# Kernel tuning notes

Hardware: AMD Instinct MI355X
Metric: run time of the kernel (lower is better)

The kernel has to match this reference:

```python
import jax, jax.numpy as jnp
import numpy as np
import math

B, L, HID = 2, 1024, 1536
NH, HD = 24, 64
DSSM = NH * HD            # 1536 (expand = 1)
QKV = 3 * DSSM
DCONV = 2
EPS = 1e-6


def _silu(u):
    return u * jax.nn.sigmoid(u)


def setup_inputs() -> dict:
    key = jax.random.key(0)
    ks = jax.random.split(key, 10)
    x = jax.random.normal(ks[0], (B, L, HID), dtype=jnp.float32)
    w_qkv = jax.random.normal(ks[1], (QKV, HID), dtype=jnp.float32) / math.sqrt(HID)
    conv_w = jax.random.normal(ks[2], (QKV, DCONV), dtype=jnp.float32) * 0.5  # depthwise causal conv, k=2
    w_dt = jax.random.normal(ks[3], (NH, HID), dtype=jnp.float32) * 0.02
    # dt_bias init exactly as in the torch module
    dt = jnp.exp(jax.random.uniform(ks[4], (NH,)) * (math.log(0.1) - math.log(0.001)) + math.log(0.001))
    dt = jnp.clip(dt, 1e-4, None)
    dt_bias = dt + jnp.log(-jnp.expm1(-dt))
    a_log = jnp.log(jax.random.uniform(ks[5], (NH,), minval=1.0, maxval=16.0))
    D = jnp.ones((NH, HD), dtype=jnp.float32)
    w_z = jax.random.normal(ks[6], (DSSM, HID), dtype=jnp.float32) / math.sqrt(HID)
    b_z = jnp.zeros((DSSM,), dtype=jnp.float32)
    rms_w = jnp.ones((DSSM,), dtype=jnp.float32)
    w_o = jax.random.normal(ks[7], (HID, DSSM), dtype=jnp.float32) / math.sqrt(DSSM)
    return dict(x=x, w_qkv=w_qkv, conv_w=conv_w, w_dt=w_dt, dt_bias=dt_bias,
                a_log=a_log, D=D, w_z=w_z, b_z=b_z, rms_w=rms_w, w_o=w_o)


def reference(x, w_qkv, conv_w, w_dt, dt_bias, a_log, D, w_z, b_z, rms_w, w_o):
    # qkv projection  [B,L,3*DSSM]
    qkv = jnp.einsum('blh,qh->blq', x, w_qkv)
    # depthwise causal conv1d (kernel size 2, padding k-1, trimmed to L)
    prev = jnp.pad(qkv, ((0, 0), (1, 0), (0, 0)))[:, :L]
    qkv = _silu(prev * conv_w[:, 0] + qkv * conv_w[:, 1])
    q, k, v = jnp.split(qkv, 3, axis=-1)
    q = q.reshape(B, L, NH, HD)
    k = k.reshape(B, L, NH, HD)
    v = v.reshape(B, L, NH, HD)
    # dt discretization: softplus(dt_proj(x) + dt_bias)   [B,L,NH]
    dt = jax.nn.softplus(jnp.einsum('blh,nh->bln', x, w_dt) + dt_bias)
    A = -jnp.exp(a_log)              # [NH], negative
    dA = dt * A                      # [B,L,NH]
    cs = jnp.transpose(jnp.cumsum(dA, axis=1), (0, 2, 1))   # [B,NH,L]
    diff = cs[:, :, :, None] - cs[:, :, None, :]            # [B,NH,L,L], <=0 on causal part
    causal = jnp.tril(jnp.ones((L, L), dtype=bool))
    decay = jnp.exp(jnp.where(causal, diff, -jnp.inf))      # segment-sum decay matrix
    # quadratic SSD (attention) form of the selective scan
    scores = jnp.einsum('bihd,bjhd->bhij', q, k) * decay
    scores = scores * jnp.transpose(dt, (0, 2, 1))[:, :, None, :]  # dt_j on keys (B-discretization)
    y = jnp.einsum('bhij,bjhd->bihd', scores, v)
    y = y + v * D                    # D skip connection
    y = y.reshape(B, L, DSSM)
    # z gate + RMSNorm + output projection
    z = jnp.einsum('blh,dh->bld', x, w_z) + b_z
    y = y * _silu(z)
    y = y * jax.lax.rsqrt(jnp.mean(y * y, axis=-1, keepdims=True) + EPS) * rms_w
    return jnp.einsum('bld,hd->blh', y, w_o)
```

## Files before the change

kernel.cpp:

```cpp
#include <hip/hip_runtime.h>
#include <hip/hip_bf16.h>
#include <math.h>

#define B_ 2
#define L_ 1024
#define HID_ 1536
#define NH_ 24
#define HD_ 64
#define DSSM_ 1536
#define QKV_ 4608
#define M_ 2048

typedef __attribute__((ext_vector_type(8))) short short8;
typedef __attribute__((ext_vector_type(4))) short short4e;
typedef __attribute__((ext_vector_type(4))) float floatx4;

__device__ __forceinline__ void gload_lds16(const short* g, short* l)
{
    __builtin_amdgcn_global_load_lds(
        (const __attribute__((address_space(1))) void*)g,
        (__attribute__((address_space(3))) void*)l,
        16, 0, 0);
}

__device__ __forceinline__ float bfs2f(short s)
{
    unsigned u = ((unsigned)(unsigned short)s) << 16;
    float f; __builtin_memcpy(&f, &u, 4); return f;
}
__device__ __forceinline__ short f2bfs(float f)
{
    __hip_bfloat16 h = __float2bfloat16(f);
    short s; __builtin_memcpy(&s, &h, 2); return s;
}

__device__ const int kIt[30] = {0,1,2,3,4,5, 6,6, 7,7, 8,8, 9,9, 10,10, 11,11,
                                12,12,12, 13,13,13, 14,14,14, 15,15,15};
__device__ const int kS[30]  = {0,0,0,0,0,0, 0,1, 0,1, 0,1, 0,1, 0,1, 0,1,
                                0,1,2, 0,1,2, 0,1,2, 0,1,2};

#define CN0 (M_ * HID_)
#define CN1 (QKV_ * HID_)
#define CN2 (DSSM_ * HID_)
#define CN3 (HID_ * DSSM_)
__global__ void cast_all_kernel(
    const float* __restrict__ x,  const float* __restrict__ wq,
    const float* __restrict__ wz, const float* __restrict__ wo,
    __hip_bfloat16* __restrict__ xb,
    __hip_bfloat16* __restrict__ wcat,
    __hip_bfloat16* __restrict__ wob)
{
    int i = (blockIdx.x * 256 + threadIdx.x) * 4;
    const float* src; __hip_bfloat16* dst; int off;
    if (i < CN0)                   { src = x;  dst = xb;         off = i; }
    else if (i < CN0 + CN1)        { src = wq; dst = wcat;       off = i - CN0; }
    else if (i < CN0 + CN1 + CN2)  { src = wz; dst = wcat + CN1; off = i - CN0 - CN1; }
    else                           { src = wo; dst = wob;        off = i - CN0 - CN1 - CN2; }
    float4 f = *reinterpret_cast<const float4*>(src + off);
    dst[off]     = __float2bfloat16(f.x);
    dst[off + 1] = __float2bfloat16(f.y);
    dst[off + 2] = __float2bfloat16(f.z);
    dst[off + 3] = __float2bfloat16(f.w);
}

#define MFMA_ __builtin_amdgcn_mfma_f32_16x16x32_bf16
#define BAR_() __builtin_amdgcn_s_barrier()

#define CSTR 200

__global__ __launch_bounds__(512, 1) void gemm_qkvz_256(
    const __hip_bfloat16* __restrict__ A,
    const __hip_bfloat16* __restrict__ Bm,
    __hip_bfloat16* __restrict__ qkv_out,
    float* __restrict__ z_out,
    const float* __restrict__ b_z)
{
    extern __shared__ short lds[];
    const int K  = HID_;
    const int NT = K / 64;
    const int tid   = threadIdx.x;
    const int lane  = tid & 63;
    const int wave  = tid >> 6;
    const int col16 = lane & 15;
    const int quad  = lane >> 4;
    const int wm = wave >> 1;
    const int wn = wave & 1;
    const int rowblk = blockIdx.y * 256;
    const int colblk = blockIdx.x * 192;

    const short* Ap = reinterpret_cast<const short*>(A);
    const short* Bp = reinterpret_cast<const short*>(Bm);

    const int o  = tid * 16;
    const int s  = o ^ (((o >> 7) & 7) << 4);
    const int sr = s >> 7;
    const int sc = (s & 127) >> 1;
    const int ldst = tid * 8;

    const int mask = (col16 & 7) << 4;
    const int e0 = ((quad * 16)      ^ mask) >> 1;
    const int e1 = ((64 + quad * 16) ^ mask) >> 1;
    const int arow = (wm * 64 + col16) * 64;
    const int brow = (wn * 96 + col16) * 64;

    floatx4 acc[4][6] = {};

    auto STAGE_A = [&](int c, int u, int t) {
        const short* g = Ap + (size_t)(rowblk + u * 64 + sr) * K + t * 64 + sc;
        gload_lds16(g, &lds[c * 16384 + u * 4096 + ldst]);
    };
    auto STAGE_B = [&](int c, int u, int t) {
        const short* g = Bp + (size_t)(colblk + u * 64 + sr) * K + t * 64 + sc;
        gload_lds16(g, &lds[32768 + c * 12288 + u * 4096 + ldst]);
    };

    STAGE_A(0, 0, 0); STAGE_A(0, 1, 0); STAGE_A(0, 2, 0); STAGE_A(0, 3, 0);
    STAGE_B(0, 0, 0); STAGE_B(0, 1, 0); STAGE_B(0, 2, 0);
    STAGE_A(1, 0, 1); STAGE_A(1, 1, 1); STAGE_A(1, 2, 1); STAGE_A(1, 3, 1);
    asm volatile("s_waitcnt vmcnt(4)" ::: "memory");
    __builtin_amdgcn_sched_barrier(0);
    BAR_();

    for (int t = 0; t < NT; ++t) {
        const int cur = t & 1, nxt = cur ^ 1;
        const int Ab = cur * 16384;
        const int Bb = 32768 + cur * 12288;
        short8 af0[4], af1[4], bf0[6], bf1[6];

#pragma unroll
        for (int m = 0; m < 4; ++m) {
            af0[m] = *reinterpret_cast<const short8*>(&lds[Ab + arow + m * 1024 + e0]);
            af1[m] = *reinterpret_cast<const short8*>(&lds[Ab + arow + m * 1024 + e1]);
        }
#pragma unroll
        for (int n = 0; n < 6; ++n) {
            bf0[n] = *reinterpret_cast<const short8*>(&lds[Bb + brow + n * 1024 + e0]);
            bf1[n] = *reinterpret_cast<const short8*>(&lds[Bb + brow + n * 1024 + e1]);
        }
        asm volatile("s_waitcnt lgkmcnt(0)" ::: "memory");
        __builtin_amdgcn_sched_barrier(0);
        BAR_();

        if (t + 1 < NT) {
            STAGE_B(nxt, 0, t + 1); STAGE_B(nxt, 1, t + 1); STAGE_B(nxt, 2, t + 1);
        }
        if (t + 2 < NT) {
            STAGE_A(cur, 0, t + 2); STAGE_A(cur, 1, t + 2);
            STAGE_A(cur, 2, t + 2); STAGE_A(cur, 3, t + 2);
        }

        __builtin_amdgcn_s_setprio(1);
#pragma unroll
        for (int m = 0; m < 4; ++m)
#pragma unroll
            for (int n = 0; n < 6; ++n) {
                acc[m][n] = MFMA_(af0[m], bf0[n], acc[m][n], 0, 0, 0);
                acc[m][n] = MFMA_(af1[m], bf1[n], acc[m][n], 0, 0, 0);
            }
        __builtin_amdgcn_s_setprio(0);

        if (t >= NT - 2) { asm volatile("s_waitcnt vmcnt(0)" ::: "memory"); }
        else             { asm volatile("s_waitcnt vmcnt(4)" ::: "memory"); }
        __builtin_amdgcn_sched_barrier(0);
        BAR_();
    }

    if (blockIdx.x < 24) {
        const int rb = wm * 64 + quad * 4;
        const int cb = wn * 96 + col16;
#pragma unroll
        for (int m = 0; m < 4; ++m)
#pragma unroll
            for (int n = 0; n < 6; ++n)
#pragma unroll
                for (int r = 0; r < 4; ++r)
                    lds[(rb + m * 16 + r) * CSTR + cb + n * 16] =
                        f2bfs(acc[m][n][r]);
        __syncthreads();
        const int row = tid >> 1;
        const int seg = tid & 1;
        const short* srcp = &lds[row * CSTR + seg * 96];
        short* dstp = reinterpret_cast<short*>(qkv_out)
                    + (size_t)(rowblk + row) * QKV_ + colblk + seg * 96;
#pragma unroll
        for (int j = 0; j < 12; ++j)
            *reinterpret_cast<short8*>(dstp + j * 8) =
                *reinterpret_cast<const short8*>(srcp + j * 8);
    } else {
        const int row0  = rowblk + wm * 64;
        const int col0g = colblk + wn * 96 - QKV_;
#pragma unroll
        for (int m = 0; m < 4; ++m)
#pragma unroll
            for (int n = 0; n < 6; ++n)
#pragma unroll
                for (int r = 0; r < 4; ++r) {
                    int row = row0 + m * 16 + quad * 4 + r;
                    int col = col0g + n * 16 + col16;
                    z_out[(size_t)row * DSSM_ + col] = acc[m][n][r] + b_z[col];
                }
    }
}

template<int OUTMODE>
__global__ __launch_bounds__(256) void gemm_nt(
    const __hip_bfloat16* __restrict__ A,
    const __hip_bfloat16* __restrict__ Bm,
    void* __restrict__ Cv,
    const float* __restrict__ bias,
    int M, int N, int K)
{
    const int lane  = threadIdx.x & 63;
    const int wave  = threadIdx.x >> 6;
    const int col16 = lane & 15;
    const int quad  = lane >> 4;
    const int wr    = wave >> 1;
    const int wc    = wave & 1;
    const int rowblk = blockIdx.y * 128;
    const int colblk = blockIdx.x * 128;

    const short* Ap = reinterpret_cast<const short*>(A);
    const short* Bp = reinterpret_cast<const short*>(Bm);

    __shared__ alignas(16) short As[128 * 32];
    __shared__ alignas(16) short Bs[128 * 32];

    const int srow = lane >> 2;
    const int scol = (lane & 3) * 8;

    floatx4 acc[4][4] = {};

    for (int k0 = 0; k0 < K; k0 += 32) {
#pragma unroll
        for (int s2 = 0; s2 < 2; ++s2) {
            const int seg = wave * 2 + s2;
            gload_lds16(Ap + (size_t)(rowblk + seg * 16 + srow) * K + k0 + scol,
                        &As[seg * 512]);
            gload_lds16(Bp + (size_t)(colblk + seg * 16 + srow) * K + k0 + scol,
                        &Bs[seg * 512]);
        }
        __syncthreads();

        short8 af[4], bf[4];
#pragma unroll
        for (int t = 0; t < 4; ++t) {
            af[t] = *reinterpret_cast<const short8*>(
                &As[(wr * 64 + t * 16 + col16) * 32 + quad * 8]);
            bf[t] = *reinterpret_cast<const short8*>(
                &Bs[(wc * 64 + t * 16 + col16) * 32 + quad * 8]);
        }
#pragma unroll
        for (int mt = 0; mt < 4; ++mt)
#pragma unroll
            for (int nt = 0; nt < 4; ++nt)
                acc[mt][nt] = __builtin_amdgcn_mfma_f32_16x16x32_bf16(
                    af[mt], bf[nt], acc[mt][nt], 0, 0, 0);
        __syncthreads();
    }

    const int row0 = rowblk + wr * 64;
    const int col0 = colblk + wc * 64;
#pragma unroll
    for (int mt = 0; mt < 4; ++mt) {
#pragma unroll
        for (int nt = 0; nt < 4; ++nt) {
#pragma unroll
            for (int r = 0; r < 4; ++r) {
                int row = row0 + mt * 16 + quad * 4 + r;
                int col = col0 + nt * 16 + col16;
                float v = acc[mt][nt][r];
                if (OUTMODE == 1) v += bias[col];
                if (OUTMODE == 2)
                    ((__hip_bfloat16*)Cv)[(size_t)row * N + col] = __float2bfloat16(v);
                else
                    ((float*)Cv)[(size_t)row * N + col] = v;
            }
        }
    }
}

__global__ void conv_silu_kernel(
    const __hip_bfloat16* __restrict__ raw,
    const float* __restrict__ conv_w,
    __hip_bfloat16* __restrict__ q,
    __hip_bfloat16* __restrict__ k,
    __hip_bfloat16* __restrict__ v)
{
    int idx8 = blockIdx.x * 256 + threadIdx.x;
    int c8 = (idx8 % (QKV_ / 8)) * 8;
    int ml = idx8 / (QKV_ / 8);
    int l  = ml % L_;
    int b  = ml / L_;

    const short* base = reinterpret_cast<const short*>(raw) + (size_t)ml * QKV_ + c8;
    short8 curv = *reinterpret_cast<const short8*>(base);
    short8 prevv = {};
    if (l > 0) prevv = *reinterpret_cast<const short8*>(base - QKV_);

    float4 w0 = *reinterpret_cast<const float4*>(conv_w + c8 * 2);
    float4 w1 = *reinterpret_cast<const float4*>(conv_w + c8 * 2 + 4);
    float4 w2 = *reinterpret_cast<const float4*>(conv_w + c8 * 2 + 8);
    float4 w3 = *reinterpret_cast<const float4*>(conv_w + c8 * 2 + 12);
    const float wa[16] = {w0.x, w0.y, w0.z, w0.w, w1.x, w1.y, w1.z, w1.w,
                          w2.x, w2.y, w2.z, w2.w, w3.x, w3.y, w3.z, w3.w};

    short8 outv;
#pragma unroll
    for (int j = 0; j < 8; ++j) {
        float u = bfs2f(prevv[j]) * wa[2 * j] + bfs2f(curv[j]) * wa[2 * j + 1];
        u = fmaxf(u, -80.f);
        outv[j] = f2bfs(u / (1.f + __expf(-u)));
    }

    int part = c8 / DSSM_;
    int cc   = c8 % DSSM_;
    int nh   = cc >> 6;
    int d    = cc & 63;
    __hip_bfloat16* dst = (part == 0) ? q : ((part == 1) ? k : v);
    *reinterpret_cast<short8*>(
        reinterpret_cast<short*>(dst) + (((size_t)b * NH_ + nh) * L_ + l) * HD_ + d)
        = outv;
}

__global__ __launch_bounds__(256) void dtproj_kernel(
    const float* __restrict__ x,
    const float* __restrict__ w_dt,
    const float* __restrict__ dt_bias,
    const float* __restrict__ a_log,
    float* __restrict__ dt,
    float* __restrict__ dA)
{
    const int tid  = threadIdx.x;
    const int wave = tid >> 6;
    const int lane = tid & 63;
    const int m0   = blockIdx.x * 8 + wave * 2;

    float4 xa[2][6];
#pragma unroll
    for (int rr = 0; rr < 2; ++rr)
#pragma unroll
        for (int j = 0; j < 6; ++j)
            xa[rr][j] = *reinterpret_cast<const float4*>(
                x + (size_t)(m0 + rr) * HID_ + lane * 4 + j * 256);

    float acc0[NH_], acc1[NH_];
#pragma unroll
    for (int n = 0; n < NH_; ++n) {
        float s0 = 0.f, s1 = 0.f;
#pragma unroll
        for (int j = 0; j < 6; ++j) {
            float4 w = *reinterpret_cast<const float4*>(
                w_dt + (size_t)n * HID_ + lane * 4 + j * 256);
            s0 += xa[0][j].x * w.x + xa[0][j].y * w.y
                + xa[0][j].z * w.z + xa[0][j].w * w.w;
            s1 += xa[1][j].x * w.x + xa[1][j].y * w.y
                + xa[1][j].z * w.z + xa[1][j].w * w.w;
        }
        acc0[n] = s0;
        acc1[n] = s1;
    }

#pragma unroll
    for (int off = 32; off; off >>= 1) {
#pragma unroll
        for (int n = 0; n < NH_; ++n) {
            acc0[n] += __shfl_xor(acc0[n], off, 64);
            acc1[n] += __shfl_xor(acc1[n], off, 64);
        }
    }

    if (lane < NH_) {
        const int n = lane;
        float bias = dt_bias[n];
        float Aval = -__expf(a_log[n]);
        float v0 = acc0[n] + bias;
        float v1 = acc1[n] + bias;
        v0 = (v0 > 20.f) ? v0 : log1pf(__expf(v0));
        v1 = (v1 > 20.f) ? v1 : log1pf(__expf(v1));
        int b0 = m0 / L_, l0 = m0 % L_;
        size_t o0 = ((size_t)b0 * NH_ + n) * L_ + l0;
        dt[o0]     = v0;
        dA[o0]     = v0 * Aval;
        dt[o0 + 1] = v1;
        dA[o0 + 1] = v1 * Aval;
    }
}

__global__ void cumsum_kernel(const float* __restrict__ dA, float* __restrict__ cs)
{
    int bnh  = blockIdx.x;
    int lane = threadIdx.x;
    const float* src = dA + (size_t)bnh * L_;
    float* dst       = cs + (size_t)bnh * L_;

    float loc[16];
    float run = 0.f;
#pragma unroll
    for (int t = 0; t < 16; ++t) { run += src[lane * 16 + t]; loc[t] = run; }
    float tot = run;
    float sc = tot;
#pragma unroll
    for (int off = 1; off < 64; off <<= 1) {
        float o = __shfl_up(sc, off, 64);
        if (lane >= off) sc += o;
    }
    float offset = sc - tot;
#pragma unroll
    for (int t = 0; t < 16; ++t) dst[lane * 16 + t] = loc[t] + offset;
}

__global__ __launch_bounds__(256) void vdt_transpose_kernel(
    const __hip_bfloat16* __restrict__ v,
    const float* __restrict__ dt,
    __hip_bfloat16* __restrict__ vt)
{
    const int lt0 = blockIdx.x * 64;
    const int bnh = blockIdx.z * NH_ + blockIdx.y;
    const int tid = threadIdx.x;

    __shared__ short T[64][72];

    {
        int row = tid >> 2;
        int cc  = (tid & 3) * 16;
        const short* sp = reinterpret_cast<const short*>(v)
                        + ((size_t)bnh * L_ + lt0 + row) * HD_ + cc;
        float dtr = dt[(size_t)bnh * L_ + lt0 + row];
        short8 a = *reinterpret_cast<const short8*>(sp);
        short8 b = *reinterpret_cast<const short8*>(sp + 8);
#pragma unroll
        for (int j = 0; j < 8; ++j) {
            T[row][cc + j]     = f2bfs(bfs2f(a[j]) * dtr);
            T[row][cc + 8 + j] = f2bfs(bfs2f(b[j]) * dtr);
        }
    }
    __syncthreads();
    {
        int d  = tid >> 2;
        int lc = (tid & 3) * 16;
        short8 o0, o1;
#pragma unroll
        for (int j = 0; j < 8; ++j) {
            o0[j] = T[lc + j][d];
            o1[j] = T[lc + 8 + j][d];
        }
        short* dst = reinterpret_cast<short*>(vt)
                   + ((size_t)bnh * HD_ + d) * L_ + lt0 + lc;
        *reinterpret_cast<short8*>(dst)     = o0;
        *reinterpret_cast<short8*>(dst + 8) = o1;
    }
}

__global__ __launch_bounds__(256) void attn_kernel(
    const __hip_bfloat16* __restrict__ q,
    const __hip_bfloat16* __restrict__ k,
    const __hip_bfloat16* __restrict__ vt,
    const float* __restrict__ cs,
    float* __restrict__ p0,
    float* __restrict__ p1,
    float* __restrict__ p2)
{
    const int pidx = blockIdx.x;
    const int it   = kIt[pidx];
    const int sl   = kS[pidx];
    const int nh   = blockIdx.y;
    const int b    = blockIdx.z;
    const int tid  = threadIdx.x;
    const int lane = tid & 63;
    const int wave = tid >> 6;
    const int col  = lane & 15;
    const int quad = lane >> 4;
    const int bnh  = b * NH_ + nh;
    const int iw0  = it * 64 + wave * 16;

    float* pout = (sl == 0) ? p0 : ((sl == 1) ? p1 : p2);

    const short* qp  = reinterpret_cast<const short*>(q);
    const short* kp  = reinterpret_cast<const short*>(k);
    const short* vtp = reinterpret_cast<const short*>(vt);

    __shared__ alignas(16) short Ks[4096];
    __shared__ alignas(16) short Ps[4 * 16 * 72];

    const short* qrow = qp + ((size_t)bnh * L_ + iw0 + col) * HD_;
    short8 aq0 = *reinterpret_cast<const short8*>(qrow + quad * 8);
    short8 aq1 = *reinterpret_cast<const short8*>(qrow + 32 + quad * 8);

    float csr[4];
#pragma unroll
    for (int r = 0; r < 4; ++r)
        csr[r] = cs[(size_t)bnh * L_ + iw0 + quad * 4 + r];

    floatx4 accO[4] = {};

    const int jt_end = min(sl * 6 + 5, it);
    for (int jt = sl * 6; jt <= jt_end; ++jt) {
        const int j0 = jt * 64;
        {
            const short* gk = kp + ((size_t)bnh * L_ + j0 + wave * 16 + (lane >> 2)) * HD_
                            + (lane & 3) * 8;
            gload_lds16(gk,      &Ks[wave * 512 + lane * 8]);
            gload_lds16(gk + 32, &Ks[2048 + wave * 512 + lane * 8]);
        }
        __syncthreads();

#pragma unroll
        for (int s = 0; s < 4; ++s) {
            int jsub = j0 + s * 16;
            if (jsub <= iw0 + 15) {
                short8 bk0 = *reinterpret_cast<const short8*>(
                    &Ks[(s * 16 + col) * 32 + quad * 8]);
                short8 bk1 = *reinterpret_cast<const short8*>(
                    &Ks[2048 + (s * 16 + col) * 32 + quad * 8]);
                floatx4 sc = {};
                sc = __builtin_amdgcn_mfma_f32_16x16x32_bf16(aq0, bk0, sc, 0, 0, 0);
                sc = __builtin_amdgcn_mfma_f32_16x16x32_bf16(aq1, bk1, sc, 0, 0, 0);
                int j = jsub + col;
                float csj = cs[(size_t)bnh * L_ + j];
#pragma unroll
                for (int r = 0; r < 4; ++r) {
                    int i = iw0 + quad * 4 + r;
                    float e = (j <= i) ? __expf(csr[r] - csj) : 0.f;
                    Ps[wave * 1152 + (quad * 4 + r) * 72 + s * 16 + col] =
                        f2bfs(sc[r] * e);
                }
            } else if (j0 + (s >> 1) * 32 <= iw0 + 15) {
#pragma unroll
                for (int r = 0; r < 4; ++r)
                    Ps[wave * 1152 + (quad * 4 + r) * 72 + s * 16 + col] = 0;
            }
        }

#pragma unroll
        for (int c = 0; c < 2; ++c) {
            if (j0 + c * 32 > iw0 + 15) continue;
            short8 pa = *reinterpret_cast<const short8*>(
                &Ps[wave * 1152 + col * 72 + c * 32 + quad * 8]);
#pragma unroll
            for (int nt = 0; nt < 4; ++nt) {
                short8 bv = *reinterpret_cast<const short8*>(
                    vtp + ((size_t)bnh * HD_ + nt * 16 + col) * L_
                        + j0 + c * 32 + quad * 8);
                accO[nt] = __builtin_amdgcn_mfma_f32_16x16x32_bf16(pa, bv, accO[nt], 0, 0, 0);
            }
        }
        __syncthreads();
    }

#pragma unroll
    for (int nt = 0; nt < 4; ++nt) {
#pragma unroll
        for (int r = 0; r < 4; ++r) {
            int i  = iw0 + quad * 4 + r;
            int dv = nt * 16 + col;
            pout[((size_t)b * L_ + i) * DSSM_ + nh * HD_ + dv] = accO[nt][r];
        }
    }
}

__global__ __launch_bounds__(256) void gate_rms_kernel(
    const float* __restrict__ p0,
    const float* __restrict__ p1,
    const float* __restrict__ p2,
    const float* __restrict__ z,
    const __hip_bfloat16* __restrict__ v,
    const float* __restrict__ Dm,
    const float* __restrict__ rms_w,
    __hip_bfloat16* __restrict__ yn)
{
    int m   = blockIdx.x;
    int b   = m / L_;
    int l   = m % L_;
    int tid = threadIdx.x;
    size_t base = (size_t)m * DSSM_;
    const bool has1 = (l >= 384);
    const bool has2 = (l >= 768);

    floatx4 acc4[2] = {};
    float ss = 0.f;
#pragma unroll
    for (int t = 0; t < 2; ++t) {
        int i4 = t * 256 + tid;
        if (i4 < DSSM_ / 4) {
            int c  = i4 * 4;
            int nh = c >> 6, d = c & 63;
            floatx4 p = *reinterpret_cast<const floatx4*>(p0 + base + c);
            if (has1) p += *reinterpret_cast<const floatx4*>(p1 + base + c);
            if (has2) p += *reinterpret_cast<const floatx4*>(p2 + base + c);
            floatx4 dm = *reinterpret_cast<const floatx4*>(Dm + c);
            floatx4 zz = *reinterpret_cast<const floatx4*>(z + base + c);
            short4e vv = *reinterpret_cast<const short4e*>(
                reinterpret_cast<const short*>(v)
                + (((size_t)b * NH_ + nh) * L_ + l) * HD_ + d);
            floatx4 g;
#pragma unroll
            for (int j = 0; j < 4; ++j) {
                float yv = p[j] + bfs2f(vv[j]) * dm[j];
                float zv = fmaxf(zz[j], -80.f);
                float gv = yv * (zv / (1.f + __expf(-zv)));
                ss += gv * gv;
                g[j] = gv;
            }
            acc4[t] = g;
        }
    }
#pragma unroll
    for (int off = 32; off; off >>= 1) ss += __shfl_xor(ss, off, 64);
    __shared__ float red[4];
    if ((tid & 63) == 0) red[tid >> 6] = ss;
    __syncthreads();
    ss = red[0] + red[1] + red[2] + red[3];
    float r = rsqrtf(ss / (float)DSSM_ + 1e-6f);
#pragma unroll
    for (int t = 0; t < 2; ++t) {
        int i4 = t * 256 + tid;
        if (i4 < DSSM_ / 4) {
            int c = i4 * 4;
            floatx4 rw = *reinterpret_cast<const floatx4*>(rms_w + c);
            short4e o;
#pragma unroll
            for (int j = 0; j < 4; ++j)
                o[j] = f2bfs(acc4[t][j] * r * rw[j]);
            *reinterpret_cast<short4e*>(
                reinterpret_cast<short*>(yn) + base + c) = o;
        }
    }
}

extern "C" void kernel_launch(void* const* d_in, const int* in_sizes, int n_in,
                              void* d_out, int out_size, void* d_ws, size_t ws_size,
                              hipStream_t stream)
{
    const float* x       = (const float*)d_in[0];
    const float* w_qkv   = (const float*)d_in[1];
    const float* conv_w  = (const float*)d_in[2];
    const float* w_dt    = (const float*)d_in[3];
    const float* dt_bias = (const float*)d_in[4];
    const float* a_log   = (const float*)d_in[5];
    const float* Dm      = (const float*)d_in[6];
    const float* w_z     = (const float*)d_in[7];
    const float* b_z     = (const float*)d_in[8];
    const float* rms_w   = (const float*)d_in[9];
    const float* w_o     = (const float*)d_in[10];
    float* out = (float*)d_out;

    char* ws = (char*)d_ws;

    __hip_bfloat16* xb    = (__hip_bfloat16*)(ws);
    __hip_bfloat16* wob   = (__hip_bfloat16*)(ws + 6291456);
    float*          zbuf  = (float*)(ws + 11010048);
    __hip_bfloat16* wcat  = (__hip_bfloat16*)(ws + 23592960);
    __hip_bfloat16* qkvb  = (__hip_bfloat16*)(ws + 42467328);
    __hip_bfloat16* qb    = (__hip_bfloat16*)(ws + 61341696);
    __hip_bfloat16* kb    = (__hip_bfloat16*)(ws + 67633152);
    __hip_bfloat16* vb    = (__hip_bfloat16*)(ws + 73924608);
    float* dt   = (float*)(ws + 80216064);
    float* dA   = (float*)(ws + 80412672);
    float* cs   = (float*)(ws + 80609280);
    __hip_bfloat16* vtb = (__hip_bfloat16*)(ws);
    __hip_bfloat16* yn  = (__hip_bfloat16*)(ws);
    float* p0 = (float*)(ws + 23592960);
    float* p1 = (float*)(ws + 36175872);
    float* p2 = (float*)(ws + 48758784);

    static bool attr_set = false;
    if (!attr_set) {
        (void)hipFuncSetAttribute(reinterpret_cast<const void*>(gemm_qkvz_256),
                                  hipFuncAttributeMaxDynamicSharedMemorySize,
                                  114688);
        attr_set = true;
    }

    cast_all_kernel<<<(CN0 + CN1 + CN2 + CN3) / 1024, 256, 0, stream>>>(
        x, w_qkv, w_z, w_o, xb, wcat, wob);

    gemm_qkvz_256<<<dim3((QKV_ + DSSM_) / 192, M_ / 256), 512, 114688, stream>>>(
        xb, wcat, qkvb, zbuf, b_z);

    conv_silu_kernel<<<(B_ * L_ * QKV_ / 8) / 256, 256, 0, stream>>>(
        qkvb, conv_w, qb, kb, vb);

    dtproj_kernel<<<M_ / 8, 256, 0, stream>>>(x, w_dt, dt_bias, a_log, dt, dA);

    cumsum_kernel<<<B_ * NH_, 64, 0, stream>>>(dA, cs);

    vdt_transpose_kernel<<<dim3(L_ / 64, NH_, B_), 256, 0, stream>>>(vb, dt, vtb);

    attn_kernel<<<dim3(30, NH_, B_), 256, 0, stream>>>(
        qb, kb, vtb, cs, p0, p1, p2);

    gate_rms_kernel<<<M_, 256, 0, stream>>>(p0, p1, p2, zbuf, vb, Dm, rms_w, yn);

    gemm_nt<0><<<dim3(HID_ / 128, M_ / 128), 256, 0, stream>>>(
        yn, wob, (void*)out, nullptr, M_, HID_, DSSM_);
}
```

Baseline: 276.2 us.

## Software-pipeline LDS fragment reads with MFMA halves in QKVZ GEMM

Restructures the QKVZ GEMM main loop so each K-tile's two 32-wide halves are read from LDS into separate register fragment sets, with the next half's LDS reads issued before the current half's MFMA cluster. A and B tiles for step t+2 are now staged together into the same buffer, and the wait counts are adjusted to match. The goal is to hide LDS read latency behind MFMA work. In exchange it adds an extra barrier per iteration and keeps two fragment sets live, which raises register pressure.

```diff
diff --git a/kernel.cpp b/kernel.cpp
--- a/kernel.cpp
+++ b/kernel.cpp
@@ -65,8 +65,32 @@
 
 #define MFMA_ __builtin_amdgcn_mfma_f32_16x16x32_bf16
 #define BAR_() __builtin_amdgcn_s_barrier()
+#define SCHED_ __builtin_amdgcn_sched_barrier(0)
 
 #define CSTR 200
+
+#define READ_FRAGS(Ab, Bb, eoff, fa, fb)                                        \
+    do {                                                                        \
+        _Pragma("unroll")                                                       \
+        for (int m_ = 0; m_ < 4; ++m_)                                          \
+            fa[m_] = *reinterpret_cast<const short8*>(                          \
+                &lds[(Ab) + arow + m_ * 1024 + (eoff)]);                        \
+        _Pragma("unroll")                                                       \
+        for (int n_ = 0; n_ < 6; ++n_)                                          \
+            fb[n_] = *reinterpret_cast<const short8*>(                          \
+                &lds[(Bb) + brow + n_ * 1024 + (eoff)]);                        \
+    } while (0)
+
+#define MFMA_CLUSTER(fa, fb)                                                    \
+    do {                                                                        \
+        __builtin_amdgcn_s_setprio(1);                                          \
+        _Pragma("unroll")                                                       \
+        for (int m_ = 0; m_ < 4; ++m_)                                          \
+            _Pragma("unroll")                                                   \
+            for (int n_ = 0; n_ < 6; ++n_)                                      \
+                acc[m_][n_] = MFMA_(fa[m_], fb[n_], acc[m_][n_], 0, 0, 0);      \
+        __builtin_amdgcn_s_setprio(0);                                          \
+    } while (0)
 
 __global__ __launch_bounds__(512, 1) void gemm_qkvz_256(
     const __hip_bfloat16* __restrict__ A,
@@ -105,64 +129,59 @@
 
     floatx4 acc[4][6] = {};
 
-    auto STAGE_A = [&](int c, int u, int t) {
-        const short* g = Ap + (size_t)(rowblk + u * 64 + sr) * K + t * 64 + sc;
-        gload_lds16(g, &lds[c * 16384 + u * 4096 + ldst]);
+    auto STAGE_ALL = [&](int c, int t) {
+        const short* ga = Ap + (size_t)(rowblk + sr) * K + t * 64 + sc;
+        short* da = &lds[c * 16384 + ldst];
+#pragma unroll
+        for (int u = 0; u < 4; ++u)
+            gload_lds16(ga + (size_t)(u * 64) * K, da + u * 4096);
+        const short* gb = Bp + (size_t)(colblk + sr) * K + t * 64 + sc;
+        short* db = &lds[32768 + c * 12288 + ldst];
+#pragma unroll
+        for (int u = 0; u < 3; ++u)
+            gload_lds16(gb + (size_t)(u * 64) * K, db + u * 4096);
     };
-    auto STAGE_B = [&](int c, int u, int t) {
-        const short* g = Bp + (size_t)(colblk + u * 64 + sr) * K + t * 64 + sc;
-        gload_lds16(g, &lds[32768 + c * 12288 + u * 4096 + ldst]);
-    };
-
-    STAGE_A(0, 0, 0); STAGE_A(0, 1, 0); STAGE_A(0, 2, 0); STAGE_A(0, 3, 0);
-    STAGE_B(0, 0, 0); STAGE_B(0, 1, 0); STAGE_B(0, 2, 0);
-    STAGE_A(1, 0, 1); STAGE_A(1, 1, 1); STAGE_A(1, 2, 1); STAGE_A(1, 3, 1);
-    asm volatile("s_waitcnt vmcnt(4)" ::: "memory");
-    __builtin_amdgcn_sched_barrier(0);
+
+    short8 fA0[4], fB0[6], fA1[4], fB1[6];
+
+    STAGE_ALL(0, 0);
+    STAGE_ALL(1, 1);
+    asm volatile("s_waitcnt vmcnt(7)" ::: "memory");
+    SCHED_;
     BAR_();
+    READ_FRAGS(0, 32768, e0, fA0, fB0);
+    asm volatile("s_waitcnt lgkmcnt(0)" ::: "memory");
+    SCHED_;
 
     for (int t = 0; t < NT; ++t) {
-        const int cur = t & 1, nxt = cur ^ 1;
+        const int cur = t & 1;
         const int Ab = cur * 16384;
         const int Bb = 32768 + cur * 12288;
-        short8 af0[4], af1[4], bf0[6], bf1[6];
-
-#pragma unroll
-        for (int m = 0; m < 4; ++m) {
-            af0[m] = *reinterpret_cast<const short8*>(&lds[Ab + arow + m * 1024 + e0]);
-            af1[m] = *reinterpret_cast<const short8*>(&lds[Ab + arow + m * 1024 + e1]);
-        }
-#pragma unroll
-        for (int n = 0; n < 6; ++n) {
-            bf0[n] = *reinterpret_cast<const short8*>(&lds[Bb + brow + n * 1024 + e0]);
-            bf1[n] = *reinterpret_cast<const short8*>(&lds[Bb + brow + n * 1024 + e1]);
-        }
+        const int Abn = (cur ^ 1) * 16384;
+        const int Bbn = 32768 + (cur ^ 1) * 12288;
+
+        READ_FRAGS(Ab, Bb, e1, fA1, fB1);
+        SCHED_;
+        MFMA_CLUSTER(fA0, fB0);
         asm volatile("s_waitcnt lgkmcnt(0)" ::: "memory");
-        __builtin_amdgcn_sched_barrier(0);
+        SCHED_;
         BAR_();
 
+        if (t + 2 < NT) STAGE_ALL(cur, t + 2);
+        if (t + 2 < NT) { asm volatile("s_waitcnt vmcnt(7)" ::: "memory"); }
+        else            { asm volatile("s_waitcnt vmcnt(0)" ::: "memory"); }
+        SCHED_;
+        BAR_();
+
         if (t + 1 < NT) {
-            STAGE_B(nxt, 0, t + 1); STAGE_B(nxt, 1, t + 1); STAGE_B(nxt, 2, t + 1);
-        }
-        if (t + 2 < NT) {
-            STAGE_A(cur, 0, t + 2); STAGE_A(cur, 1, t + 2);
-            STAGE_A(cur, 2, t + 2); STAGE_A(cur, 3, t + 2);
-        }
-
-        __builtin_amdgcn_s_setprio(1);
-#pragma unroll
-        for (int m = 0; m < 4; ++m)
-#pragma unroll
-            for (int n = 0; n < 6; ++n) {
-                acc[m][n] = MFMA_(af0[m], bf0[n], acc[m][n], 0, 0, 0);
-                acc[m][n] = MFMA_(af1[m], bf1[n], acc[m][n], 0, 0, 0);
-            }
-        __builtin_amdgcn_s_setprio(0);
-
-        if (t >= NT - 2) { asm volatile("s_waitcnt vmcnt(0)" ::: "memory"); }
-        else             { asm volatile("s_waitcnt vmcnt(4)" ::: "memory"); }
-        __builtin_amdgcn_sched_barrier(0);
-        BAR_();
+            READ_FRAGS(Abn, Bbn, e0, fA0, fB0);
+            SCHED_;
+        }
+        MFMA_CLUSTER(fA1, fB1);
+        if (t + 1 < NT) {
+            asm volatile("s_waitcnt lgkmcnt(0)" ::: "memory");
+            SCHED_;
+        }
     }
 
     if (blockIdx.x < 24) {
```

New measurement: 279.6 us. About the same (+1.2%).

## Retile QKVZ GEMM to 128-row blocks and drop attention key-split partials

Applied to the files above, without the earlier changes.

The QKV/Z projection GEMM moves from 256-row tiles with 512 threads and one block per CU to 128-row tiles with 256 threads and two blocks per CU. A and B staging is merged into one simpler double-buffered prefetch that waits for all loads before each barrier. The attention kernel no longer splits key tiles across up to three blocks writing separate partial buffers; each block handles a full query tile and launches longest tiles first. This removes the extra partial-buffer writes and the summation in the gate/RMS kernel, at the cost of fewer, more unbalanced attention blocks and a shallower GEMM prefetch pipeline.

```diff
diff --git a/kernel.cpp b/kernel.cpp
--- a/kernel.cpp
+++ b/kernel.cpp
@@ -33,11 +33,6 @@
     __hip_bfloat16 h = __float2bfloat16(f);
     short s; __builtin_memcpy(&s, &h, 2); return s;
 }
-
-__device__ const int kIt[30] = {0,1,2,3,4,5, 6,6, 7,7, 8,8, 9,9, 10,10, 11,11,
-                                12,12,12, 13,13,13, 14,14,14, 15,15,15};
-__device__ const int kS[30]  = {0,0,0,0,0,0, 0,1, 0,1, 0,1, 0,1, 0,1, 0,1,
-                                0,1,2, 0,1,2, 0,1,2, 0,1,2};
 
 #define CN0 (M_ * HID_)
 #define CN1 (QKV_ * HID_)
@@ -65,10 +60,11 @@
 
 #define MFMA_ __builtin_amdgcn_mfma_f32_16x16x32_bf16
 #define BAR_() __builtin_amdgcn_s_barrier()
+#define SCHED_ __builtin_amdgcn_sched_barrier(0)
 
 #define CSTR 200
 
-__global__ __launch_bounds__(512, 1) void gemm_qkvz_256(
+__global__ __launch_bounds__(256, 2) void gemm_qkvz_128(
     const __hip_bfloat16* __restrict__ A,
     const __hip_bfloat16* __restrict__ Bm,
     __hip_bfloat16* __restrict__ qkv_out,
@@ -85,7 +81,7 @@
     const int quad  = lane >> 4;
     const int wm = wave >> 1;
     const int wn = wave & 1;
-    const int rowblk = blockIdx.y * 256;
+    const int rowblk = blockIdx.y * 128;
     const int colblk = blockIdx.x * 192;
 
     const short* Ap = reinterpret_cast<const short*>(A);
@@ -95,7 +91,6 @@
     const int s  = o ^ (((o >> 7) & 7) << 4);
     const int sr = s >> 7;
     const int sc = (s & 127) >> 1;
-    const int ldst = tid * 8;
 
     const int mask = (col16 & 7) << 4;
     const int e0 = ((quad * 16)      ^ mask) >> 1;
@@ -105,28 +100,31 @@
 
     floatx4 acc[4][6] = {};
 
-    auto STAGE_A = [&](int c, int u, int t) {
-        const short* g = Ap + (size_t)(rowblk + u * 64 + sr) * K + t * 64 + sc;
-        gload_lds16(g, &lds[c * 16384 + u * 4096 + ldst]);
+    auto STAGE_ALL = [&](int c, int t) {
+        const short* ga = Ap + (size_t)(rowblk + sr) * K + t * 64 + sc;
+        short* da = &lds[c * 8192 + tid * 8];
+#pragma unroll
+        for (int u = 0; u < 4; ++u)
+            gload_lds16(ga + (size_t)(u * 32) * K, da + u * 2048);
+        const short* gb = Bp + (size_t)(colblk + sr) * K + t * 64 + sc;
+        short* db = &lds[16384 + c * 12288 + tid * 8];
+#pragma unroll
+        for (int u = 0; u < 6; ++u)
+            gload_lds16(gb + (size_t)(u * 32) * K, db + u * 2048);
     };
-    auto STAGE_B = [&](int c, int u, int t) {
-        const short* g = Bp + (size_t)(colblk + u * 64 + sr) * K + t * 64 + sc;
-        gload_lds16(g, &lds[32768 + c * 12288 + u * 4096 + ldst]);
-    };
-
-    STAGE_A(0, 0, 0); STAGE_A(0, 1, 0); STAGE_A(0, 2, 0); STAGE_A(0, 3, 0);
-    STAGE_B(0, 0, 0); STAGE_B(0, 1, 0); STAGE_B(0, 2, 0);
-    STAGE_A(1, 0, 1); STAGE_A(1, 1, 1); STAGE_A(1, 2, 1); STAGE_A(1, 3, 1);
-    asm volatile("s_waitcnt vmcnt(4)" ::: "memory");
-    __builtin_amdgcn_sched_barrier(0);
+
+    STAGE_ALL(0, 0);
+    asm volatile("s_waitcnt vmcnt(0)" ::: "memory");
+    SCHED_;
     BAR_();
 
     for (int t = 0; t < NT; ++t) {
-        const int cur = t & 1, nxt = cur ^ 1;
-        const int Ab = cur * 16384;
-        const int Bb = 32768 + cur * 12288;
+        const int cur = t & 1;
+        if (t + 1 < NT) STAGE_ALL(cur ^ 1, t + 1);
+
+        const int Ab = cur * 8192;
+        const int Bb = 16384 + cur * 12288;
         short8 af0[4], af1[4], bf0[6], bf1[6];
-
 #pragma unroll
         for (int m = 0; m < 4; ++m) {
             af0[m] = *reinterpret_cast<const short8*>(&lds[Ab + arow + m * 1024 + e0]);
@@ -138,16 +136,7 @@
             bf1[n] = *reinterpret_cast<const short8*>(&lds[Bb + brow + n * 1024 + e1]);
         }
         asm volatile("s_waitcnt lgkmcnt(0)" ::: "memory");
-        __builtin_amdgcn_sched_barrier(0);
-        BAR_();
-
-        if (t + 1 < NT) {
-            STAGE_B(nxt, 0, t + 1); STAGE_B(nxt, 1, t + 1); STAGE_B(nxt, 2, t + 1);
-        }
-        if (t + 2 < NT) {
-            STAGE_A(cur, 0, t + 2); STAGE_A(cur, 1, t + 2);
-            STAGE_A(cur, 2, t + 2); STAGE_A(cur, 3, t + 2);
-        }
+        SCHED_;
 
         __builtin_amdgcn_s_setprio(1);
 #pragma unroll
@@ -159,9 +148,8 @@
             }
         __builtin_amdgcn_s_setprio(0);
 
-        if (t >= NT - 2) { asm volatile("s_waitcnt vmcnt(0)" ::: "memory"); }
-        else             { asm volatile("s_waitcnt vmcnt(4)" ::: "memory"); }
-        __builtin_amdgcn_sched_barrier(0);
+        asm volatile("s_waitcnt vmcnt(0)" ::: "memory");
+        SCHED_;
         BAR_();
     }
 
@@ -456,13 +444,9 @@
     const __hip_bfloat16* __restrict__ k,
     const __hip_bfloat16* __restrict__ vt,
     const float* __restrict__ cs,
-    float* __restrict__ p0,
-    float* __restrict__ p1,
-    float* __restrict__ p2)
-{
-    const int pidx = blockIdx.x;
-    const int it   = kIt[pidx];
-    const int sl   = kS[pidx];
+    float* __restrict__ p0)
+{
+    const int it   = 15 - blockIdx.x;
     const int nh   = blockIdx.y;
     const int b    = blockIdx.z;
     const int tid  = threadIdx.x;
@@ -473,8 +457,6 @@
     const int bnh  = b * NH_ + nh;
     const int iw0  = it * 64 + wave * 16;
 
-    float* pout = (sl == 0) ? p0 : ((sl == 1) ? p1 : p2);
-
     const short* qp  = reinterpret_cast<const short*>(q);
     const short* kp  = reinterpret_cast<const short*>(k);
     const short* vtp = reinterpret_cast<const short*>(vt);
@@ -493,8 +475,7 @@
 
     floatx4 accO[4] = {};
 
-    const int jt_end = min(sl * 6 + 5, it);
-    for (int jt = sl * 6; jt <= jt_end; ++jt) {
+    for (int jt = 0; jt <= it; ++jt) {
         const int j0 = jt * 64;
         {
             const short* gk = kp + ((size_t)bnh * L_ + j0 + wave * 16 + (lane >> 2)) * HD_
@@ -553,15 +534,13 @@
         for (int r = 0; r < 4; ++r) {
             int i  = iw0 + quad * 4 + r;
             int dv = nt * 16 + col;
-            pout[((size_t)b * L_ + i) * DSSM_ + nh * HD_ + dv] = accO[nt][r];
+            p0[((size_t)b * L_ + i) * DSSM_ + nh * HD_ + dv] = accO[nt][r];
         }
     }
 }
 
 __global__ __launch_bounds__(256) void gate_rms_kernel(
     const float* __restrict__ p0,
-    const float* __restrict__ p1,
-    const float* __restrict__ p2,
     const float* __restrict__ z,
     const __hip_bfloat16* __restrict__ v,
     const float* __restrict__ Dm,
@@ -573,8 +552,6 @@
     int l   = m % L_;
     int tid = threadIdx.x;
     size_t base = (size_t)m * DSSM_;
-    const bool has1 = (l >= 384);
-    const bool has2 = (l >= 768);
 
     floatx4 acc4[2] = {};
     float ss = 0.f;
@@ -585,8 +562,6 @@
             int c  = i4 * 4;
             int nh = c >> 6, d = c & 63;
             floatx4 p = *reinterpret_cast<const floatx4*>(p0 + base + c);
-            if (has1) p += *reinterpret_cast<const floatx4*>(p1 + base + c);
-            if (has2) p += *reinterpret_cast<const floatx4*>(p2 + base + c);
             floatx4 dm = *reinterpret_cast<const floatx4*>(Dm + c);
             floatx4 zz = *reinterpret_cast<const floatx4*>(z + base + c);
             short4e vv = *reinterpret_cast<const short4e*>(
@@ -660,21 +635,19 @@
     __hip_bfloat16* vtb = (__hip_bfloat16*)(ws);
     __hip_bfloat16* yn  = (__hip_bfloat16*)(ws);
     float* p0 = (float*)(ws + 23592960);
-    float* p1 = (float*)(ws + 36175872);
-    float* p2 = (float*)(ws + 48758784);
 
     static bool attr_set = false;
     if (!attr_set) {
-        (void)hipFuncSetAttribute(reinterpret_cast<const void*>(gemm_qkvz_256),
+        (void)hipFuncSetAttribute(reinterpret_cast<const void*>(gemm_qkvz_128),
                                   hipFuncAttributeMaxDynamicSharedMemorySize,
-                                  114688);
+                                  81920);
         attr_set = true;
     }
 
     cast_all_kernel<<<(CN0 + CN1 + CN2 + CN3) / 1024, 256, 0, stream>>>(
         x, w_qkv, w_z, w_o, xb, wcat, wob);
 
-    gemm_qkvz_256<<<dim3((QKV_ + DSSM_) / 192, M_ / 256), 512, 114688, stream>>>(
+    gemm_qkvz_128<<<dim3((QKV_ + DSSM_) / 192, M_ / 128), 256, 81920, stream>>>(
         xb, wcat, qkvb, zbuf, b_z);
 
     conv_silu_kernel<<<(B_ * L_ * QKV_ / 8) / 256, 256, 0, stream>>>(
@@ -686,10 +659,10 @@
 
     vdt_transpose_kernel<<<dim3(L_ / 64, NH_, B_), 256, 0, stream>>>(vb, dt, vtb);
 
-    attn_kernel<<<dim3(30, NH_, B_), 256, 0, stream>>>(
-        qb, kb, vtb, cs, p0, p1, p2);
-
-    gate_rms_kernel<<<M_, 256, 0, stream>>>(p0, p1, p2, zbuf, vb, Dm, rms_w, yn);
+    attn_kernel<<<dim3(16, NH_, B_), 256, 0, stream>>>(
+        qb, kb, vtb, cs, p0);
+
+    gate_rms_kernel<<<M_, 256, 0, stream>>>(p0, zbuf, vb, Dm, rms_w, yn);
 
     gemm_nt<0><<<dim3(HID_ / 128, M_ / 128), 256, 0, stream>>>(
         yn, wob, (void*)out, nullptr, M_, HID_, DSSM_);
```

Measured after the change: 294.1 us. 6.5% more time.
